# Optimization experiments

Hardware: AMD Instinct MI355X
Metric: run time of the kernel (lower is better)

The kernel has to match this reference:

```python
import jax, jax.numpy as jnp
import numpy as np

D_MODEL = 1024
NUM_HEADS = 16
D_HEAD = D_MODEL // NUM_HEADS


def setup_inputs() -> dict:
    key = jax.random.key(0)
    ks = jax.random.split(key, 8)
    B, S = 2, 2048
    query_x = jax.random.normal(ks[0], (B, S, D_MODEL), dtype=jnp.float32)
    key_x = jax.random.normal(ks[1], (B, S, D_MODEL), dtype=jnp.float32)
    value_x = jax.random.normal(ks[2], (B, S, D_MODEL), dtype=jnp.float32)
    mask = jnp.zeros((S, S), dtype=jnp.float32)  # additive mask, broadcast over B,H
    scale = np.sqrt(2.0 / D_MODEL)  # kaiming-ish init
    w_query = jax.random.normal(ks[3], (D_MODEL, D_MODEL), dtype=jnp.float32) * scale
    w_key = jax.random.normal(ks[4], (D_MODEL, D_MODEL), dtype=jnp.float32) * scale
    w_value = jax.random.normal(ks[5], (D_MODEL, D_MODEL), dtype=jnp.float32) * scale
    w0 = jax.random.normal(ks[6], (D_MODEL, D_MODEL), dtype=jnp.float32) * scale
    return {"query_x": query_x, "key_x": key_x, "value_x": value_x, "mask": mask,
            "w_query": w_query, "w_key": w_key, "w_value": w_value, "w0": w0}


def reference(query_x, key_x, value_x, mask, w_query, w_key, w_value, w0):
    B, S, _ = query_x.shape
    # nn.Linear applies x @ W.T; weights stored [out, in]
    def proj(x, w):
        y = jnp.einsum('bsd,ed->bse', x, w)              # [B,S,D]
        return y.reshape(B, S, NUM_HEADS, D_HEAD).transpose(0, 2, 1, 3)  # [B,H,S,Dh]
    q = proj(query_x, w_query)
    k = proj(key_x, w_key)
    v = proj(value_x, w_value)
    scores = jnp.einsum('bhqd,bhkd->bhqk', q, k) / jnp.sqrt(jnp.float32(D_HEAD))
    scores = scores + mask  # broadcast additive mask
    attn = jax.nn.softmax(scores, axis=-1)
    out = jnp.einsum('bhqk,bhkd->bhqd', attn, v)         # [B,H,S,Dh]
    out = out.transpose(0, 2, 1, 3).reshape(B, S, NUM_HEADS * D_HEAD)
    return jnp.einsum('bsd,ed->bse', out, w0)
```

## Files before the change

kernel.cpp:

```cpp
#include <hip/hip_runtime.h>
#include <hip/hip_bf16.h>
#include <stdint.h>

#define D_MODEL 1024
#define NH 16
#define DH 64
#define SEQ 2048
#define MROWS 4096
#define LOG2E 1.44269504088896340736f

typedef unsigned short ushort_t;
typedef __attribute__((ext_vector_type(4))) float f32x4;
typedef __attribute__((ext_vector_type(16))) float f32x16;
typedef __attribute__((ext_vector_type(4))) unsigned short us4;
typedef __attribute__((ext_vector_type(8))) unsigned short us8;
typedef __attribute__((ext_vector_type(4))) unsigned int u32x4;
typedef __attribute__((ext_vector_type(8))) __bf16 bf16x8;

__device__ __forceinline__ f32x4 mfma16(us8 a, us8 b, f32x4 c) {
    return __builtin_amdgcn_mfma_f32_16x16x32_bf16(
        __builtin_bit_cast(bf16x8, a), __builtin_bit_cast(bf16x8, b), c, 0, 0, 0);
}
__device__ __forceinline__ f32x16 mfma32(us8 a, us8 b, f32x16 c) {
    return __builtin_amdgcn_mfma_f32_32x32x16_bf16(
        __builtin_bit_cast(bf16x8, a), __builtin_bit_cast(bf16x8, b), c, 0, 0, 0);
}

__device__ __forceinline__ ushort_t f2bf(float f) {
    union { float f; uint32_t u; } v; v.f = f;
    uint32_t r = v.u + 0x7fffu + ((v.u >> 16) & 1u);
    return (ushort_t)(r >> 16);
}

__device__ __forceinline__ unsigned int cvtpk(float lo, float hi) {
    unsigned int r;
    asm("v_cvt_pk_bf16_f32 %0, %1, %2" : "=v"(r) : "v"(lo), "v"(hi));
    return r;
}

__device__ __forceinline__ float exp2_fast(float x) {
#if __has_builtin(__builtin_amdgcn_exp2f)
    return __builtin_amdgcn_exp2f(x);
#else
    float r; asm("v_exp_f32 %0, %1" : "=v"(r) : "v"(x)); return r;
#endif
}

__device__ __forceinline__ void gload16(const void* g, void* l) {
    __builtin_amdgcn_global_load_lds(
        (const __attribute__((address_space(1))) void*)g,
        (__attribute__((address_space(3))) void*)l, 16, 0, 0);
}

__global__ __launch_bounds__(256) void conv_multi(
    const float* __restrict__ s0, ushort_t* __restrict__ d0,
    const float* __restrict__ s1, ushort_t* __restrict__ d1,
    const float* __restrict__ s2, ushort_t* __restrict__ d2,
    const float* __restrict__ s3, ushort_t* __restrict__ d3, int n4)
{
    int z = blockIdx.z;
    const float* s = z == 0 ? s0 : z == 1 ? s1 : z == 2 ? s2 : s3;
    ushort_t* d    = z == 0 ? d0 : z == 1 ? d1 : z == 2 ? d2 : d3;
    int i = blockIdx.x * 256 + threadIdx.x;
    int stride = gridDim.x * 256;
    for (; i < n4; i += stride) {
        float4 v = ((const float4*)s)[i];
        us4 o;
        o[0] = f2bf(v.x); o[1] = f2bf(v.y); o[2] = f2bf(v.z); o[3] = f2bf(v.w);
        ((us4*)d)[i] = o;
    }
}

__global__ __launch_bounds__(256) void mask_flags(const float* __restrict__ mask,
                                                  int* __restrict__ flags)
{
    int qt = blockIdx.x, kt = blockIdx.y;
    int t = threadIdx.x;
    bool nz = false;
#pragma unroll
    for (int i = 0; i < 4; i++) {
        int idx = t + i * 256;
        int row = idx >> 4, c4 = (idx & 15) * 4;
        float4 v = *(const float4*)(mask + (size_t)(qt * 64 + row) * SEQ + kt * 64 + c4);
        nz |= (v.x != 0.f) | (v.y != 0.f) | (v.z != 0.f) | (v.w != 0.f);
    }
    if (__any((int)nz) && (t & 63) == 0) atomicOr(&flags[qt * 32 + kt], 1);
}

__device__ __forceinline__ void gemm_stage(const ushort_t* __restrict__ A,
                                           const ushort_t* __restrict__ B,
                                           int m0, int n0, int t, int w, int k0,
                                           ushort_t* sA, ushort_t* sB)
{
#pragma unroll
    for (int r = 0; r < 4; r++) {
        int chunk = r * 256 + t;
        int row = chunk >> 3, c8 = (chunk & 7) * 8;
        gload16(A + (size_t)(m0 + row) * D_MODEL + k0 + c8,
                &sA[(r * 256 + w * 64) * 8]);
    }
#pragma unroll
    for (int r = 0; r < 2; r++) {
        int chunk = r * 256 + t;
        int row = chunk >> 3, c8 = (chunk & 7) * 8;
        gload16(B + (size_t)(n0 + row) * D_MODEL + k0 + c8,
                &sB[(r * 256 + w * 64) * 8]);
    }
}

__device__ __forceinline__ void gemm_core(const ushort_t* __restrict__ A,
                                          const ushort_t* __restrict__ B,
                                          int m0, int n0, int t,
                                          ushort_t* sA, ushort_t* sB,
                                          f32x4 acc[4][2])
{
    const int lane = t & 63, w = t >> 6;
    const int lr = lane & 15, lg = lane >> 4;
    const int wm = (w >> 1) * 64, wn = (w & 1) * 32;

    gemm_stage(A, B, m0, n0, t, w, 0, sA, sB);
    __syncthreads();

    for (int it = 0; it < D_MODEL / 64; ++it) {
        const int cur = it & 1;
        const ushort_t* cA = sA + cur * (128 * 64);
        const ushort_t* cB = sB + cur * (64 * 64);

        us8 af[4][2], bfr[2][2];
#pragma unroll
        for (int i = 0; i < 4; i++)
#pragma unroll
            for (int ks = 0; ks < 2; ks++)
                af[i][ks] = *(const us8*)&cA[(wm + i * 16 + lr) * 64 + ks * 32 + 8 * lg];
#pragma unroll
        for (int j = 0; j < 2; j++)
#pragma unroll
            for (int ks = 0; ks < 2; ks++)
                bfr[j][ks] = *(const us8*)&cB[(wn + j * 16 + lr) * 64 + ks * 32 + 8 * lg];

        if (it + 1 < D_MODEL / 64)
            gemm_stage(A, B, m0, n0, t, w, (it + 1) * 64,
                       sA + (cur ^ 1) * (128 * 64), sB + (cur ^ 1) * (64 * 64));

#pragma unroll
        for (int i = 0; i < 4; i++)
#pragma unroll
            for (int j = 0; j < 2; j++)
#pragma unroll
                for (int ks = 0; ks < 2; ks++)
                    acc[i][j] = mfma16(af[i][ks], bfr[j][ks], acc[i][j]);

        __syncthreads();
    }
}

__global__ __launch_bounds__(256) void gemm_qk(const ushort_t* __restrict__ A0,
                                               const ushort_t* __restrict__ A1,
                                               const ushort_t* __restrict__ Wq,
                                               const ushort_t* __restrict__ Wk,
                                               ushort_t* __restrict__ Qo,
                                               ushort_t* __restrict__ Ko)
{
    __shared__ ushort_t sA[2][128 * 64];
    __shared__ ushort_t sB[2][64 * 64];
    const int z = blockIdx.z;
    const ushort_t* A = z ? A1 : A0;
    const ushort_t* W = z ? Wk : Wq;
    ushort_t* C = z ? Ko : Qo;
    const float scale = z ? 1.0f : 0.125f * LOG2E;
    const int t = threadIdx.x, lane = t & 63, w = t >> 6;
    const int lr = lane & 15, lg = lane >> 4;
    const int wm = (w >> 1) * 64, wn = (w & 1) * 32;
    const int m0 = blockIdx.x * 128, n0 = blockIdx.y * 64;

    f32x4 acc[4][2];
    f32x4 zero = {0.f, 0.f, 0.f, 0.f};
#pragma unroll
    for (int i = 0; i < 4; i++)
#pragma unroll
        for (int j = 0; j < 2; j++) acc[i][j] = zero;
    gemm_core(A, W, m0, n0, t, &sA[0][0], &sB[0][0], acc);

#pragma unroll
    for (int i = 0; i < 4; i++)
#pragma unroll
        for (int j = 0; j < 2; j++)
#pragma unroll
            for (int r = 0; r < 4; r++) {
                int m = m0 + wm + i * 16 + 4 * lg + r;
                int n = n0 + wn + j * 16 + lr;
                int b = m >> 11, s = m & 2047;
                int h = n >> 6, dh = n & 63;
                C[(((size_t)(b * NH + h)) * SEQ + s) * DH + dh] = f2bf(acc[i][j][r] * scale);
            }
}

__global__ __launch_bounds__(256) void gemm_v(const ushort_t* __restrict__ A,
                                              const ushort_t* __restrict__ W,
                                              ushort_t* __restrict__ VT)
{
    __shared__ ushort_t sA[2][128 * 64];
    __shared__ ushort_t sB[2][64 * 64];
    const int t = threadIdx.x, lane = t & 63, w = t >> 6;
    const int lr = lane & 15, lg = lane >> 4;
    const int wm = (w >> 1) * 64, wn = (w & 1) * 32;
    const int m0 = blockIdx.x * 128, n0 = blockIdx.y * 64;

    f32x4 acc[4][2];
    f32x4 zero = {0.f, 0.f, 0.f, 0.f};
#pragma unroll
    for (int i = 0; i < 4; i++)
#pragma unroll
        for (int j = 0; j < 2; j++) acc[i][j] = zero;
    gemm_core(A, W, m0, n0, t, &sA[0][0], &sB[0][0], acc);

#pragma unroll
    for (int i = 0; i < 4; i++)
#pragma unroll
        for (int j = 0; j < 2; j++) {
            int m = m0 + wm + i * 16 + 4 * lg;
            int n = n0 + wn + j * 16 + lr;
            int b = m >> 11, s = m & 2047;
            int h = n >> 6, dh = n & 63;
            us4 o;
#pragma unroll
            for (int r = 0; r < 4; r++) o[r] = f2bf(acc[i][j][r]);
            *(us4*)&VT[(((size_t)(b * NH + h)) * DH + dh) * SEQ + s] = o;
        }
}

__global__ __launch_bounds__(256) void gemm_o(const ushort_t* __restrict__ A,
                                              const ushort_t* __restrict__ W,
                                              float* __restrict__ C)
{
    __shared__ ushort_t sA[2][128 * 64];
    __shared__ ushort_t sB[2][64 * 64];
    const int t = threadIdx.x, lane = t & 63, w = t >> 6;
    const int lr = lane & 15, lg = lane >> 4;
    const int wm = (w >> 1) * 64, wn = (w & 1) * 32;
    const int m0 = blockIdx.x * 128, n0 = blockIdx.y * 64;

    f32x4 acc[4][2];
    f32x4 zero = {0.f, 0.f, 0.f, 0.f};
#pragma unroll
    for (int i = 0; i < 4; i++)
#pragma unroll
        for (int j = 0; j < 2; j++) acc[i][j] = zero;
    gemm_core(A, W, m0, n0, t, &sA[0][0], &sB[0][0], acc);

#pragma unroll
    for (int i = 0; i < 4; i++)
#pragma unroll
        for (int j = 0; j < 2; j++)
#pragma unroll
            for (int r = 0; r < 4; r++) {
                int m = m0 + wm + i * 16 + 4 * lg + r;
                int n = n0 + wn + j * 16 + lr;
                C[(size_t)m * D_MODEL + n] = acc[i][j][r];
            }
}

__global__ __launch_bounds__(256, 2) void attn_fwd(const ushort_t* __restrict__ Q,
                                                   const ushort_t* __restrict__ K,
                                                   const ushort_t* __restrict__ VT,
                                                   const float* __restrict__ mask,
                                                   const int* __restrict__ flags,
                                                   ushort_t* __restrict__ O)
{
    __shared__ ushort_t sK[2][128 * 64];
    __shared__ ushort_t sVT[2][64 * 128];

    const int t = threadIdx.x, lane = t & 63, w = t >> 6;
    const int l31 = lane & 31, lh = lane >> 5;
    const int id = blockIdx.x;
    const int bh = (id & 7) * 4 + ((id >> 3) >> 4);
    const int qt = (id >> 3) & 15;
    const int b = bh >> 4, h = bh & 15;
    const int q = qt * 128 + w * 32 + l31;

    unsigned long long blt = __ballot(flags[(qt * 2 + lh) * 32 + l31] != 0);
    const unsigned int fl = (unsigned int)(blt | (blt >> 32));

    us8 qfr[4];
#pragma unroll
    for (int ks = 0; ks < 4; ks++)
        qfr[ks] = *(const us8*)(Q + ((size_t)bh * SEQ + q) * DH + ks * 16 + 8 * lh);

    f32x16 acc_o[2];
#pragma unroll
    for (int d = 0; d < 2; d++)
#pragma unroll
        for (int r = 0; r < 16; r++) acc_o[d][r] = 0.f;
    float acc_l = 0.f;

    const ushort_t* Kb = K + (size_t)bh * SEQ * DH;
    const ushort_t* Vb = VT + (size_t)bh * DH * SEQ;

#define STAGE(kvt_, buf_)                                                     \
    {                                                                         \
        _Pragma("unroll")                                                     \
        for (int r = 0; r < 4; r++) {                                         \
            int j = r * 256 + t;                                              \
            int row = j >> 3, cc = (j & 7) ^ (row & 7);                       \
            gload16(Kb + (size_t)((kvt_) * 128 + row) * DH + cc * 8,          \
                    &sK[buf_][(r * 256 + w * 64) * 8]);                       \
        }                                                                     \
        _Pragma("unroll")                                                     \
        for (int r = 0; r < 4; r++) {                                         \
            int j = r * 256 + t;                                              \
            int row = j >> 4, cc = (j & 15) ^ (row & 15);                     \
            gload16(Vb + (size_t)row * SEQ + (kvt_) * 128 + cc * 8,           \
                    &sVT[buf_][(r * 256 + w * 64) * 8]);                      \
        }                                                                     \
    }

    STAGE(0, 0);
    __syncthreads();

    for (int kvt = 0; kvt < SEQ / 128; ++kvt) {
        const int cur = kvt & 1;
        const char* cK = (const char*)sK[cur];
        const char* cV = (const char*)sVT[cur];

        f32x16 sacc[4];
#pragma unroll
        for (int kb = 0; kb < 4; kb++)
#pragma unroll
            for (int r = 0; r < 16; r++) sacc[kb][r] = 0.f;
        __builtin_amdgcn_s_setprio(1);
#pragma unroll
        for (int ks = 0; ks < 4; ks++)
#pragma unroll
            for (int kb = 0; kb < 4; kb++) {
                int row = kb * 32 + l31;
                int by = (row * 128 + (ks * 16 + 8 * lh) * 2) ^ ((row & 7) << 4);
                us8 kf = *(const us8*)(cK + by);
                sacc[kb] = mfma32(kf, qfr[ks], sacc[kb]);
            }
        __builtin_amdgcn_s_setprio(0);

        if (kvt + 1 < SEQ / 128) STAGE(kvt + 1, cur ^ 1);

#pragma unroll
        for (int hf = 0; hf < 2; hf++) {
            us8 vf[4][2];
#pragma unroll
            for (int ks = 0; ks < 4; ks++)
#pragma unroll
                for (int dblk = 0; dblk < 2; dblk++) {
                    int row = dblk * 32 + l31;
                    int by = (row * 256 + hf * 128 + ks * 32 + 16 * lh)
                             ^ ((row & 15) << 4);
                    vf[ks][dblk] = *(const us8*)(cV + by);
                }

            if ((fl >> (2 * kvt + hf)) & 1u) {
#pragma unroll
                for (int kk = 0; kk < 2; kk++) {
                    const int kb = 2 * hf + kk;
#pragma unroll
                    for (int r = 0; r < 16; r++) {
                        int kcol = kb * 32 + (r & 3) + 8 * (r >> 2) + 4 * lh;
                        sacc[kb][r] += mask[(size_t)q * SEQ + kvt * 128 + kcol] * LOG2E;
                    }
                }
            }

            float rs = 0.f;
#pragma unroll
            for (int kk = 0; kk < 2; kk++)
#pragma unroll
                for (int r = 0; r < 16; r++) {
                    float p = exp2_fast(sacc[2 * hf + kk][r]);
                    sacc[2 * hf + kk][r] = p;
                    rs += p;
                }
            rs += __shfl_xor(rs, 32);
            acc_l += rs;

            __builtin_amdgcn_s_setprio(1);
#pragma unroll
            for (int ks = 0; ks < 4; ks++) {
                const int kb = 2 * hf + (ks >> 1), u = ks & 1;
                unsigned int W0 = cvtpk(sacc[kb][8 * u + 0], sacc[kb][8 * u + 1]);
                unsigned int W1 = cvtpk(sacc[kb][8 * u + 2], sacc[kb][8 * u + 3]);
                unsigned int W2 = cvtpk(sacc[kb][8 * u + 4], sacc[kb][8 * u + 5]);
                unsigned int W3 = cvtpk(sacc[kb][8 * u + 6], sacc[kb][8 * u + 7]);
                asm("v_permlane32_swap_b32 %0, %1" : "+v"(W0), "+v"(W2));
                asm("v_permlane32_swap_b32 %0, %1" : "+v"(W1), "+v"(W3));
                u32x4 pw;
                pw[0] = W0; pw[1] = W1; pw[2] = W2; pw[3] = W3;
                us8 pf = __builtin_bit_cast(us8, pw);
#pragma unroll
                for (int dblk = 0; dblk < 2; dblk++)
                    acc_o[dblk] = mfma32(vf[ks][dblk], pf, acc_o[dblk]);
            }
            __builtin_amdgcn_s_setprio(0);
        }

        __syncthreads();
    }

    float inv = 1.f / acc_l;
    ushort_t* Orow = O + ((size_t)(b * SEQ) + q) * D_MODEL + h * DH;
#pragma unroll
    for (int dblk = 0; dblk < 2; dblk++)
#pragma unroll
        for (int g = 0; g < 4; g++) {
            unsigned int lo = cvtpk(acc_o[dblk][4 * g + 0] * inv,
                                    acc_o[dblk][4 * g + 1] * inv);
            unsigned int hi = cvtpk(acc_o[dblk][4 * g + 2] * inv,
                                    acc_o[dblk][4 * g + 3] * inv);
            uint2 pr; pr.x = lo; pr.y = hi;
            *(uint2*)(Orow + dblk * 32 + 8 * g + 4 * lh) = pr;
        }
#undef STAGE
}

extern "C" void kernel_launch(void* const* d_in, const int* in_sizes, int n_in,
                              void* d_out, int out_size, void* d_ws, size_t ws_size,
                              hipStream_t stream)
{
    const float* qx   = (const float*)d_in[0];
    const float* kx   = (const float*)d_in[1];
    const float* vx   = (const float*)d_in[2];
    const float* mask = (const float*)d_in[3];
    const float* wq   = (const float*)d_in[4];
    const float* wk   = (const float*)d_in[5];
    const float* wv   = (const float*)d_in[6];
    const float* w0   = (const float*)d_in[7];
    float* out = (float*)d_out;

    char* ws = (char*)d_ws;
    const size_t MB = 1024 * 1024;
    ushort_t* A0 = (ushort_t*)(ws);
    ushort_t* A1 = (ushort_t*)(ws + 8 * MB);
    ushort_t* Wq = (ushort_t*)(ws + 16 * MB);
    ushort_t* Wk = (ushort_t*)(ws + 18 * MB);
    ushort_t* Wv = (ushort_t*)(ws + 20 * MB);
    ushort_t* W0 = (ushort_t*)(ws + 22 * MB);
    ushort_t* VT = (ushort_t*)(ws + 24 * MB);
    int* flags   = (int*)(ws + 32 * MB);
    ushort_t* AO = A1;
    ushort_t* Qb = (ushort_t*)d_out;
    ushort_t* Kb = (ushort_t*)d_out + 4 * MB;

    hipMemsetAsync(flags, 0, 32 * 32 * sizeof(int), stream);
    mask_flags<<<dim3(32, 32), 256, 0, stream>>>(mask, flags);

    conv_multi<<<dim3(256, 1, 4), 256, 0, stream>>>(wq, Wq, wk, Wk, wv, Wv, w0, W0, 262144);
    conv_multi<<<dim3(1024, 1, 2), 256, 0, stream>>>(qx, A0, kx, A1, qx, A0, qx, A0, 1048576);

    gemm_qk<<<dim3(32, 16, 2), 256, 0, stream>>>(A0, A1, Wq, Wk, Qb, Kb);

    conv_multi<<<dim3(1024, 1, 1), 256, 0, stream>>>(vx, A0, vx, A0, vx, A0, vx, A0, 1048576);
    gemm_v<<<dim3(32, 16), 256, 0, stream>>>(A0, Wv, VT);

    attn_fwd<<<512, 256, 0, stream>>>(Qb, Kb, VT, mask, flags, AO);

    gemm_o<<<dim3(32, 16), 256, 0, stream>>>(AO, W0, out);
}
```

Measured before the change: 143.0 us.

## Compute softmax row sums via MFMA with ones, use hardware bf16 packing

The attention kernel now accumulates the softmax denominator with an extra MFMA that multiplies the bf16-rounded probabilities by a ones vector, replacing the per-element VALU adds and the cross-lane shuffle. The sum is now taken over the same bf16 values that feed the PV product, so normalization matches the numerator. The conversion and GEMM epilogue kernels replace the software round-to-nearest bf16 routine with the v_cvt_pk_bf16_f32 instruction. K/V staging addresses are precomputed once per thread instead of recomputed every tile. The extra MFMA adds matrix-unit work and 16 accumulator registers per thread, which could raise register pressure.

```diff
diff --git a/kernel.cpp b/kernel.cpp
--- a/kernel.cpp
+++ b/kernel.cpp
@@ -26,16 +26,13 @@
         __builtin_bit_cast(bf16x8, a), __builtin_bit_cast(bf16x8, b), c, 0, 0, 0);
 }
 
-__device__ __forceinline__ ushort_t f2bf(float f) {
-    union { float f; uint32_t u; } v; v.f = f;
-    uint32_t r = v.u + 0x7fffu + ((v.u >> 16) & 1u);
-    return (ushort_t)(r >> 16);
-}
-
 __device__ __forceinline__ unsigned int cvtpk(float lo, float hi) {
     unsigned int r;
     asm("v_cvt_pk_bf16_f32 %0, %1, %2" : "=v"(r) : "v"(lo), "v"(hi));
     return r;
+}
+__device__ __forceinline__ ushort_t f2bf1(float f) {
+    return (ushort_t)(cvtpk(f, f) & 0xffffu);
 }
 
 __device__ __forceinline__ float exp2_fast(float x) {
@@ -65,9 +62,10 @@
     int stride = gridDim.x * 256;
     for (; i < n4; i += stride) {
         float4 v = ((const float4*)s)[i];
-        us4 o;
-        o[0] = f2bf(v.x); o[1] = f2bf(v.y); o[2] = f2bf(v.z); o[3] = f2bf(v.w);
-        ((us4*)d)[i] = o;
+        uint2 pr;
+        pr.x = cvtpk(v.x, v.y);
+        pr.y = cvtpk(v.z, v.w);
+        ((uint2*)d)[i] = pr;
     }
 }
 
@@ -191,7 +189,7 @@
                 int n = n0 + wn + j * 16 + lr;
                 int b = m >> 11, s = m & 2047;
                 int h = n >> 6, dh = n & 63;
-                C[(((size_t)(b * NH + h)) * SEQ + s) * DH + dh] = f2bf(acc[i][j][r] * scale);
+                C[(((size_t)(b * NH + h)) * SEQ + s) * DH + dh] = f2bf1(acc[i][j][r] * scale);
             }
 }
 
@@ -222,10 +220,10 @@
             int n = n0 + wn + j * 16 + lr;
             int b = m >> 11, s = m & 2047;
             int h = n >> 6, dh = n & 63;
-            us4 o;
-#pragma unroll
-            for (int r = 0; r < 4; r++) o[r] = f2bf(acc[i][j][r]);
-            *(us4*)&VT[(((size_t)(b * NH + h)) * DH + dh) * SEQ + s] = o;
+            uint2 pr;
+            pr.x = cvtpk(acc[i][j][0], acc[i][j][1]);
+            pr.y = cvtpk(acc[i][j][2], acc[i][j][3]);
+            *(uint2*)&VT[(((size_t)(b * NH + h)) * DH + dh) * SEQ + s] = pr;
         }
 }
 
@@ -286,32 +284,42 @@
     for (int ks = 0; ks < 4; ks++)
         qfr[ks] = *(const us8*)(Q + ((size_t)bh * SEQ + q) * DH + ks * 16 + 8 * lh);
 
-    f32x16 acc_o[2];
+    f32x16 acc_o[2], acc_lv;
 #pragma unroll
     for (int d = 0; d < 2; d++)
 #pragma unroll
         for (int r = 0; r < 16; r++) acc_o[d][r] = 0.f;
-    float acc_l = 0.f;
+#pragma unroll
+    for (int r = 0; r < 16; r++) acc_lv[r] = 0.f;
+
+    us8 ones;
+#pragma unroll
+    for (int i = 0; i < 8; i++) ones[i] = 0x3F80;
 
     const ushort_t* Kb = K + (size_t)bh * SEQ * DH;
     const ushort_t* Vb = VT + (size_t)bh * DH * SEQ;
+
+    const ushort_t* kp[4];
+    const ushort_t* vp[4];
+#pragma unroll
+    for (int r = 0; r < 4; r++) {
+        int j = r * 256 + t;
+        int rowK = j >> 3, ccK = (j & 7) ^ (rowK & 7);
+        kp[r] = Kb + (size_t)rowK * DH + ccK * 8;
+        int rowV = j >> 4, ccV = (j & 15) ^ (rowV & 15);
+        vp[r] = Vb + (size_t)rowV * SEQ + ccV * 8;
+    }
 
 #define STAGE(kvt_, buf_)                                                     \
     {                                                                         \
         _Pragma("unroll")                                                     \
-        for (int r = 0; r < 4; r++) {                                         \
-            int j = r * 256 + t;                                              \
-            int row = j >> 3, cc = (j & 7) ^ (row & 7);                       \
-            gload16(Kb + (size_t)((kvt_) * 128 + row) * DH + cc * 8,          \
+        for (int r = 0; r < 4; r++)                                           \
+            gload16(kp[r] + (size_t)(kvt_) * (128 * DH),                      \
                     &sK[buf_][(r * 256 + w * 64) * 8]);                       \
-        }                                                                     \
         _Pragma("unroll")                                                     \
-        for (int r = 0; r < 4; r++) {                                         \
-            int j = r * 256 + t;                                              \
-            int row = j >> 4, cc = (j & 15) ^ (row & 15);                     \
-            gload16(Vb + (size_t)row * SEQ + (kvt_) * 128 + cc * 8,           \
+        for (int r = 0; r < 4; r++)                                           \
+            gload16(vp[r] + (size_t)(kvt_) * 128,                             \
                     &sVT[buf_][(r * 256 + w * 64) * 8]);                      \
-        }                                                                     \
     }
 
     STAGE(0, 0);
@@ -366,17 +374,11 @@
                 }
             }
 
-            float rs = 0.f;
 #pragma unroll
             for (int kk = 0; kk < 2; kk++)
 #pragma unroll
-                for (int r = 0; r < 16; r++) {
-                    float p = exp2_fast(sacc[2 * hf + kk][r]);
-                    sacc[2 * hf + kk][r] = p;
-                    rs += p;
-                }
-            rs += __shfl_xor(rs, 32);
-            acc_l += rs;
+                for (int r = 0; r < 16; r++)
+                    sacc[2 * hf + kk][r] = exp2_fast(sacc[2 * hf + kk][r]);
 
             __builtin_amdgcn_s_setprio(1);
 #pragma unroll
@@ -391,6 +393,7 @@
                 u32x4 pw;
                 pw[0] = W0; pw[1] = W1; pw[2] = W2; pw[3] = W3;
                 us8 pf = __builtin_bit_cast(us8, pw);
+                acc_lv = mfma32(ones, pf, acc_lv);
 #pragma unroll
                 for (int dblk = 0; dblk < 2; dblk++)
                     acc_o[dblk] = mfma32(vf[ks][dblk], pf, acc_o[dblk]);
@@ -401,7 +404,7 @@
         __syncthreads();
     }
 
-    float inv = 1.f / acc_l;
+    float inv = 1.f / acc_lv[0];
     ushort_t* Orow = O + ((size_t)(b * SEQ) + q) * D_MODEL + h * DH;
 #pragma unroll
     for (int dblk = 0; dblk < 2; dblk++)
```

Result: no change. 145.7 us (+1.8%).
